# Kernel tuning notes

Measured on AMD Instinct MI355X. Metric: run time of the kernel, lower is better.

The kernel has to match this reference:

```python
import jax, jax.numpy as jnp
import numpy as np

N = 100_000          # nodes
E = 3_200_000        # train edges (avg degree 32)
E_TEST = 500_000     # pos/neg test edges each
F_IN, F_HID, F_OUT = 256, 16, 64


def setup_inputs() -> dict:
    key = jax.random.key(0)
    ks = jax.random.split(key, 7)
    x = jax.random.normal(ks[0], (N, F_IN), jnp.float32)
    train_edge_index = jax.random.randint(ks[1], (2, E), 0, N, dtype=jnp.int32)
    test_pos_edge_index = jax.random.randint(ks[2], (2, E_TEST), 0, N, dtype=jnp.int32)
    test_neg_edge_index = jax.random.randint(ks[3], (2, E_TEST), 0, N, dtype=jnp.int32)
    W1 = jax.random.normal(ks[4], (F_IN, F_HID), jnp.float32) / np.float32(np.sqrt(F_IN))
    b1 = jnp.zeros((F_HID,), jnp.float32)
    W2 = jax.random.normal(ks[5], (F_HID, F_OUT), jnp.float32) / np.float32(np.sqrt(F_HID))
    b2 = jnp.zeros((F_OUT,), jnp.float32)
    return dict(x=x, train_edge_index=train_edge_index,
                test_pos_edge_index=test_pos_edge_index,
                test_neg_edge_index=test_neg_edge_index,
                W1=W1, b1=b1, W2=W2, b2=b2)


def gcn_conv(x, edge_index, W, b, n):
    """PyG GCNConv: x' = D^-1/2 (A+I) D^-1/2 (x W) + b (self-loops added)."""
    h = x @ W                                  # project first (PyG order)
    loop = jnp.arange(n, dtype=edge_index.dtype)
    src = jnp.concatenate([edge_index[0], loop])
    dst = jnp.concatenate([edge_index[1], loop])
    deg = jax.ops.segment_sum(jnp.ones_like(dst, dtype=h.dtype), dst, num_segments=n)
    dinv = jnp.where(deg > 0, jax.lax.rsqrt(deg), 0.0)
    norm = dinv[src] * dinv[dst]               # per-edge symmetric norm
    msg = h[src] * norm[:, None]               # gather + scale
    out = jax.ops.segment_sum(msg, dst, num_segments=n)  # scatter-add
    return out + b


def reference(x, train_edge_index, test_pos_edge_index, test_neg_edge_index,
              W1, b1, W2, b2):
    n = x.shape[0]
    z = gcn_conv(x, train_edge_index, W1, b1, n)
    z = jax.nn.relu(z)
    z = gcn_conv(z, train_edge_index, W2, b2, n)
    edge_index = jnp.concatenate([test_pos_edge_index, test_neg_edge_index], axis=-1)
    logits = jnp.sum(z[edge_index[0]] * z[edge_index[1]], axis=-1)
    return logits
```

## Files before the change

### kernel.cpp

```cpp
#include <hip/hip_runtime.h>


#define NB_SHIFT 8
#define CAP   9728
#define CHUNK 8192

__global__ void seedprep_kernel(int* __restrict__ gtail, int nb1,
                                const float* __restrict__ W2, const float* __restrict__ b2,
                                float* __restrict__ mw) {
    int t = threadIdx.x;
    for (int i = t; i < nb1; i += 256) gtail[i] = i * CAP;
    int r = t >> 4, cc = t & 15;
    float s = 0.0f;
    for (int j = 0; j < 64; ++j) s += W2[r * 64 + j] * W2[cc * 64 + j];
    mw[t] = s;
    if (t < 16) {
        float w = 0.0f;
        for (int j = 0; j < 64; ++j) w += W2[t * 64 + j] * b2[j];
        mw[256 + t] = w;
    }
    if (t == 0) {
        float bbv = 0.0f;
        for (int j = 0; j < 64; ++j) bbv += b2[j] * b2[j];
        mw[272] = bbv;
    }
}

__global__ void __launch_bounds__(512)
passA1_kernel(const int* __restrict__ src, const int* __restrict__ dst, int E,
              int* __restrict__ gtail, unsigned* __restrict__ tmp, int nb1) {
    __shared__ int h[512];
    __shared__ int loff[512];
    __shared__ int cur[512];
    __shared__ int base[512];
    __shared__ unsigned srec[CHUNK];
    __shared__ unsigned short sbkt[CHUNK];
    int t = threadIdx.x;
    int c0 = blockIdx.x * CHUNK;
    int ce = min(CHUNK, E - c0);

    h[t] = 0;
    __syncthreads();
    for (int i = t; i < ce; i += 512)
        atomicAdd(&h[dst[c0 + i] >> NB_SHIFT], 1);
    __syncthreads();
    int cnt = h[t];
    loff[t] = cnt;
    __syncthreads();
    for (int off = 1; off < 512; off <<= 1) {
        int v = loff[t];
        int a = (t >= off) ? loff[t - off] : 0;
        __syncthreads();
        loff[t] = v + a;
        __syncthreads();
    }
    int excl = loff[t] - cnt;
    if (t < nb1) base[t] = atomicAdd(&gtail[t], cnt);
    loff[t] = excl;
    cur[t]  = excl;
    __syncthreads();
    for (int i = t; i < ce; i += 512) {
        int d = dst[c0 + i];
        int s = src[c0 + i];
        int b = d >> NB_SHIFT;
        int p = atomicAdd(&cur[b], 1);
        srec[p] = (unsigned)s | ((unsigned)(d & 255) << 20);
        sbkt[p] = (unsigned short)b;
    }
    __syncthreads();
    for (int i = t; i < ce; i += 512) {
        int b = sbkt[i];
        tmp[base[b] + (i - loff[b])] = srec[i];
    }
}

__global__ void __launch_bounds__(512)
fill2_kernel(const int* __restrict__ gtail, const unsigned* __restrict__ tmp,
             int* __restrict__ eidx, int* __restrict__ rowptr,
             int* __restrict__ counts, float* __restrict__ dinv, int n) {
    __shared__ int hh[256];
    __shared__ int sc[256];
    __shared__ int cur[256];
    __shared__ int sout[CAP];
    int b = blockIdx.x;
    int t = threadIdx.x;
    int beg = b * CAP;
    int cnt_total = gtail[b] - beg;

    if (t < 256) hh[t] = 0;
    __syncthreads();
    for (int i = t; i < cnt_total; i += 512)
        atomicAdd(&hh[tmp[beg + i] >> 20], 1);
    __syncthreads();
    if (t < 256) sc[t] = hh[t];
    __syncthreads();
    for (int off = 1; off < 256; off <<= 1) {
        int v = 0, a = 0;
        if (t < 256) { v = sc[t]; a = (t >= off) ? sc[t - off] : 0; }
        __syncthreads();
        if (t < 256) sc[t] = v + a;
        __syncthreads();
    }
    if (t < 256) {
        int ex = sc[t] - hh[t];
        cur[t] = ex;
        int v = (b << NB_SHIFT) + t;
        if (v < n) {
            rowptr[v] = beg + ex;
            counts[v] = hh[t];
            dinv[v]   = rsqrtf((float)hh[t] + 1.0f);
        }
    }
    __syncthreads();
    for (int i = t; i < cnt_total; i += 512) {
        unsigned r = tmp[beg + i];
        int p = atomicAdd(&cur[r >> 20], 1);
        sout[p] = (int)(r & 0xFFFFF);
    }
    __syncthreads();
    for (int i = t; i < cnt_total; i += 512)
        eidx[beg + i] = sout[i];
}

__global__ void __launch_bounds__(64)
gemm1_kernel(const float* __restrict__ x, const float* __restrict__ W1,
             const float* __restrict__ dinv, float* __restrict__ hs, int n) {
    int row = blockIdx.x * 64 + threadIdx.x;
    if (row >= n) return;
    const float4* x4 = (const float4*)(x + (size_t)row * 256);
    const float4* W14 = (const float4*)W1;
    float4 a0 = {0,0,0,0}, a1 = {0,0,0,0}, a2 = {0,0,0,0}, a3 = {0,0,0,0};
    float4 buf[8];
    #pragma unroll
    for (int j = 0; j < 8; ++j) buf[j] = x4[j];
    for (int k8 = 0; k8 < 8; ++k8) {
        float4 cur[8];
        #pragma unroll
        for (int j = 0; j < 8; ++j) cur[j] = buf[j];
        if (k8 < 7) {
            #pragma unroll
            for (int j = 0; j < 8; ++j) buf[j] = x4[(k8 + 1) * 8 + j];
        }
        #pragma unroll
        for (int jj = 0; jj < 8; ++jj) {
            float4 xv = cur[jj];
            int k4 = k8 * 8 + jj;
            #pragma unroll
            for (int j = 0; j < 4; ++j) {
                float xk = (j == 0) ? xv.x : (j == 1) ? xv.y : (j == 2) ? xv.z : xv.w;
                int k = (k4 << 2) + j;
                float4 w0 = W14[k * 4 + 0];
                float4 w1 = W14[k * 4 + 1];
                float4 w2 = W14[k * 4 + 2];
                float4 w3 = W14[k * 4 + 3];
                a0.x += xk * w0.x; a0.y += xk * w0.y; a0.z += xk * w0.z; a0.w += xk * w0.w;
                a1.x += xk * w1.x; a1.y += xk * w1.y; a1.z += xk * w1.z; a1.w += xk * w1.w;
                a2.x += xk * w2.x; a2.y += xk * w2.y; a2.z += xk * w2.z; a2.w += xk * w2.w;
                a3.x += xk * w3.x; a3.y += xk * w3.y; a3.z += xk * w3.z; a3.w += xk * w3.w;
            }
        }
    }
    float di = dinv[row];
    float4* o = (float4*)(hs + (size_t)row * 16);
    a0.x *= di; a0.y *= di; a0.z *= di; a0.w *= di;
    a1.x *= di; a1.y *= di; a1.z *= di; a1.w *= di;
    a2.x *= di; a2.y *= di; a2.z *= di; a2.w *= di;
    a3.x *= di; a3.y *= di; a3.z *= di; a3.w *= di;
    o[0] = a0; o[1] = a1; o[2] = a2; o[3] = a3;
}

__global__ void agg1_kernel(const int* __restrict__ rowptr, const int* __restrict__ counts,
                            const int* __restrict__ eidx, const float4* __restrict__ hs4,
                            const float* __restrict__ dinv, const float* __restrict__ b1,
                            float4* __restrict__ gs4, int n) {
    int t = blockIdx.x * blockDim.x + threadIdx.x;
    int v = t >> 3;
    if (v >= n) return;
    int q = t & 3, hh = (t >> 2) & 1;
    int start = rowptr[v], cnt = counts[v];
    float4 s = {0, 0, 0, 0};
    int i = hh;
    for (; i + 6 < cnt; i += 8) {
        int s0 = eidx[start + i];
        int s1 = eidx[start + i + 2];
        int s2 = eidx[start + i + 4];
        int s3 = eidx[start + i + 6];
        float4 h0 = hs4[(size_t)s0 * 4 + q];
        float4 h1 = hs4[(size_t)s1 * 4 + q];
        float4 h2 = hs4[(size_t)s2 * 4 + q];
        float4 h3 = hs4[(size_t)s3 * 4 + q];
        s.x += h0.x + h1.x + h2.x + h3.x;
        s.y += h0.y + h1.y + h2.y + h3.y;
        s.z += h0.z + h1.z + h2.z + h3.z;
        s.w += h0.w + h1.w + h2.w + h3.w;
    }
    for (; i < cnt; i += 2) {
        float4 h0 = hs4[(size_t)eidx[start + i] * 4 + q];
        s.x += h0.x; s.y += h0.y; s.z += h0.z; s.w += h0.w;
    }
    s.x += __shfl_xor(s.x, 4);
    s.y += __shfl_xor(s.y, 4);
    s.z += __shfl_xor(s.z, 4);
    s.w += __shfl_xor(s.w, 4);
    if (hh == 0) {
        float di = dinv[v];
        float4 h = hs4[(size_t)v * 4 + q];
        float4 b = ((const float4*)b1)[q];
        float4 z;
        z.x = fmaxf(di * (s.x + h.x) + b.x, 0.0f) * di;
        z.y = fmaxf(di * (s.y + h.y) + b.y, 0.0f) * di;
        z.z = fmaxf(di * (s.z + h.z) + b.z, 0.0f) * di;
        z.w = fmaxf(di * (s.w + h.w) + b.w, 0.0f) * di;
        gs4[(size_t)v * 4 + q] = z;
    }
}

__global__ void agg2y_kernel(const int* __restrict__ rowptr, const int* __restrict__ counts,
                             const int* __restrict__ eidx, const float4* __restrict__ gs4,
                             const float* __restrict__ dinv, const float* __restrict__ mw,
                             float4* __restrict__ u4, float* __restrict__ y,
                             float* __restrict__ c, int n) {
    __shared__ float su[32 * 16];
    __shared__ float sM[256];
    __shared__ float sw[16];
    int t = threadIdx.x;
    sM[t] = mw[t];
    if (t < 16) sw[t] = mw[256 + t];

    int j = t >> 3, q = t & 3, hh = (t >> 2) & 1;
    int v = blockIdx.x * 32 + j;
    if (v < n) {
        int start = rowptr[v], cnt = counts[v];
        float4 s = {0, 0, 0, 0};
        int i = hh;
        for (; i + 6 < cnt; i += 8) {
            int s0 = eidx[start + i];
            int s1 = eidx[start + i + 2];
            int s2 = eidx[start + i + 4];
            int s3 = eidx[start + i + 6];
            float4 g0 = gs4[(size_t)s0 * 4 + q];
            float4 g1 = gs4[(size_t)s1 * 4 + q];
            float4 g2 = gs4[(size_t)s2 * 4 + q];
            float4 g3 = gs4[(size_t)s3 * 4 + q];
            s.x += g0.x + g1.x + g2.x + g3.x;
            s.y += g0.y + g1.y + g2.y + g3.y;
            s.z += g0.z + g1.z + g2.z + g3.z;
            s.w += g0.w + g1.w + g2.w + g3.w;
        }
        for (; i < cnt; i += 2) {
            float4 g0 = gs4[(size_t)eidx[start + i] * 4 + q];
            s.x += g0.x; s.y += g0.y; s.z += g0.z; s.w += g0.w;
        }
        s.x += __shfl_xor(s.x, 4);
        s.y += __shfl_xor(s.y, 4);
        s.z += __shfl_xor(s.z, 4);
        s.w += __shfl_xor(s.w, 4);
        if (hh == 0) {
            float di = dinv[v];
            float4 g = gs4[(size_t)v * 4 + q];
            float4 uu;
            uu.x = di * (s.x + g.x);
            uu.y = di * (s.y + g.y);
            uu.z = di * (s.z + g.z);
            uu.w = di * (s.w + g.w);
            float* up = &su[j * 16 + q * 4];
            up[0] = uu.x; up[1] = uu.y; up[2] = uu.z; up[3] = uu.w;
            u4[(size_t)v * 4 + q] = uu;
        }
    }
    __syncthreads();
    if (v < n) {
        int l8 = t & 7;
        const float* uu = &su[j * 16];
        int c0 = l8 * 2;
        float y0 = sw[c0], y1 = sw[c0 + 1];
        #pragma unroll
        for (int k = 0; k < 16; ++k) {
            float uk = uu[k];
            y0 += uk * sM[k * 16 + c0];
            y1 += uk * sM[k * 16 + c0 + 1];
        }
        float2* yp = (float2*)(y + (size_t)v * 16 + c0);
        *yp = make_float2(y0, y1);
        if (l8 == 0) {
            float cv = 0.0f;
            #pragma unroll
            for (int k = 0; k < 16; ++k) cv += uu[k] * sw[k];
            c[v] = cv;
        }
    }
}

__global__ void edge_dot_kernel(const int* __restrict__ pa, const int* __restrict__ pb,
                                const int* __restrict__ na, const int* __restrict__ nb_,
                                int ET, const float* __restrict__ u, const float* __restrict__ y,
                                const float* __restrict__ c, const float* __restrict__ mw,
                                float* __restrict__ out) {
    int t = blockIdx.x * blockDim.x + threadIdx.x;
    int p = t >> 4, l = t & 15;
    if (p >= ET) return;
    int a0 = pa[p], b0 = pb[p];
    int a1 = na[p], b1 = nb_[p];
    float ya0 = y[(size_t)a0 * 16 + l];
    float ub0 = u[(size_t)b0 * 16 + l];
    float ya1 = y[(size_t)a1 * 16 + l];
    float ub1 = u[(size_t)b1 * 16 + l];
    float p0 = ya0 * ub0;
    float p1 = ya1 * ub1;
    p0 += __shfl_xor(p0, 1);  p1 += __shfl_xor(p1, 1);
    p0 += __shfl_xor(p0, 2);  p1 += __shfl_xor(p1, 2);
    p0 += __shfl_xor(p0, 4);  p1 += __shfl_xor(p1, 4);
    p0 += __shfl_xor(p0, 8);  p1 += __shfl_xor(p1, 8);
    if (l == 0) {
        float bb = mw[272];
        out[p]      = p0 + c[a0] + bb;
        out[ET + p] = p1 + c[a1] + bb;
    }
}

extern "C" void kernel_launch(void* const* d_in, const int* in_sizes, int n_in,
                              void* d_out, int out_size, void* d_ws, size_t ws_size,
                              hipStream_t stream) {
    const float* x    = (const float*)d_in[0];
    const int*   tei  = (const int*)d_in[1];
    const int*   tpos = (const int*)d_in[2];
    const int*   tneg = (const int*)d_in[3];
    const float* W1   = (const float*)d_in[4];
    const float* b1   = (const float*)d_in[5];
    const float* W2   = (const float*)d_in[6];
    const float* b2   = (const float*)d_in[7];
    float* out = (float*)d_out;

    int n   = in_sizes[0] / 256;
    int E   = in_sizes[1] / 2;
    int ET  = in_sizes[2] / 2;
    int nb1 = (n + 255) >> NB_SHIFT;

    char* w = (char*)d_ws;
    int*   gtail  = (int*)w;        w += 512 * 4;
    float* mw     = (float*)w;      w += 512 * 4;
    int*   rowptr = (int*)w;        w += (size_t)n * 4;
    int*   counts = (int*)w;        w += (size_t)n * 4;
    float* dinv   = (float*)w;      w += (size_t)n * 4;
    float* hs     = (float*)w;      w += (size_t)16 * n * 4;
    float* gs     = (float*)w;      w += (size_t)16 * n * 4;
    float* u      = (float*)w;      w += (size_t)16 * n * 4;
    float* y      = (float*)w;      w += (size_t)16 * n * 4;
    float* c      = (float*)w;      w += (size_t)n * 4;
    int*   eidx   = (int*)w;        w += (size_t)nb1 * CAP * 4;
    unsigned* tmp = (unsigned*)w;   w += (size_t)nb1 * CAP * 4;

    const int* src = tei;
    const int* dst = tei + E;

    seedprep_kernel<<<1, 256, 0, stream>>>(gtail, nb1, W2, b2, mw);
    passA1_kernel<<<(E + CHUNK - 1) / CHUNK, 512, 0, stream>>>(src, dst, E, gtail, tmp, nb1);
    fill2_kernel<<<nb1, 512, 0, stream>>>(gtail, tmp, eidx, rowptr, counts, dinv, n);

    gemm1_kernel<<<(n + 63) / 64, 64, 0, stream>>>(x, W1, dinv, hs, n);
    agg1_kernel<<<(8 * n + 255) / 256, 256, 0, stream>>>(rowptr, counts, eidx,
                                                         (const float4*)hs, dinv, b1,
                                                         (float4*)gs, n);
    agg2y_kernel<<<(n + 31) / 32, 256, 0, stream>>>(rowptr, counts, eidx,
                                                    (const float4*)gs, dinv, mw,
                                                    (float4*)u, y, c, n);
    edge_dot_kernel<<<(16 * ET + 255) / 256, 256, 0, stream>>>(tpos, tpos + ET, tneg, tneg + ET,
                                                               ET, u, y, c, mw, out);
}
```

Before: 349.6 us.

## Fuse dense projection into edge bucketing launch and defer dinv scaling to fill

The x@W1 projection no longer needs dinv, so it moves into the same launch as the edge bucketing pass, using separate block ranges so the bandwidth-heavy GEMM runs alongside the atomic-heavy partitioning. The dinv row scaling of hs moves to the end of fill2, where each block rescales its 256 rows in place using dinv values kept in shared memory. This removes one kernel launch and lets the two independent phases overlap. The cost is that GEMM blocks now use 512 threads and inherit the large shared-memory footprint of the partitioning blocks, which limits occupancy, and fill2 gains an extra read-modify-write pass over hs.

```diff
diff --git a/kernel.cpp b/kernel.cpp
--- a/kernel.cpp
+++ b/kernel.cpp
@@ -26,17 +26,60 @@
     }
 }
 
-__global__ void __launch_bounds__(512)
-passA1_kernel(const int* __restrict__ src, const int* __restrict__ dst, int E,
-              int* __restrict__ gtail, unsigned* __restrict__ tmp, int nb1) {
+__global__ void __launch_bounds__(512, 4)
+k1_kernel(const int* __restrict__ src, const int* __restrict__ dst, int E,
+          int* __restrict__ gtail, unsigned* __restrict__ tmp, int nb1,
+          const float* __restrict__ x, const float* __restrict__ W1,
+          float* __restrict__ hs, int n, int nblkG) {
+    int t = threadIdx.x;
+    if ((int)blockIdx.x < nblkG) {
+        int row = blockIdx.x * 512 + t;
+        if (row >= n) return;
+        const float4* x4 = (const float4*)(x + (size_t)row * 256);
+        const float4* W14 = (const float4*)W1;
+        float4 a0 = {0,0,0,0}, a1 = {0,0,0,0}, a2 = {0,0,0,0}, a3 = {0,0,0,0};
+        float4 buf[8];
+        #pragma unroll
+        for (int j = 0; j < 8; ++j) buf[j] = x4[j];
+        for (int k8 = 0; k8 < 8; ++k8) {
+            float4 cur[8];
+            #pragma unroll
+            for (int j = 0; j < 8; ++j) cur[j] = buf[j];
+            if (k8 < 7) {
+                #pragma unroll
+                for (int j = 0; j < 8; ++j) buf[j] = x4[(k8 + 1) * 8 + j];
+            }
+            #pragma unroll
+            for (int jj = 0; jj < 8; ++jj) {
+                float4 xv = cur[jj];
+                int k4 = k8 * 8 + jj;
+                #pragma unroll
+                for (int j = 0; j < 4; ++j) {
+                    float xk = (j == 0) ? xv.x : (j == 1) ? xv.y : (j == 2) ? xv.z : xv.w;
+                    int k = (k4 << 2) + j;
+                    float4 w0 = W14[k * 4 + 0];
+                    float4 w1 = W14[k * 4 + 1];
+                    float4 w2 = W14[k * 4 + 2];
+                    float4 w3 = W14[k * 4 + 3];
+                    a0.x += xk * w0.x; a0.y += xk * w0.y; a0.z += xk * w0.z; a0.w += xk * w0.w;
+                    a1.x += xk * w1.x; a1.y += xk * w1.y; a1.z += xk * w1.z; a1.w += xk * w1.w;
+                    a2.x += xk * w2.x; a2.y += xk * w2.y; a2.z += xk * w2.z; a2.w += xk * w2.w;
+                    a3.x += xk * w3.x; a3.y += xk * w3.y; a3.z += xk * w3.z; a3.w += xk * w3.w;
+                }
+            }
+        }
+        float4* o = (float4*)(hs + (size_t)row * 16);
+        o[0] = a0; o[1] = a1; o[2] = a2; o[3] = a3;
+        return;
+    }
+
     __shared__ int h[512];
     __shared__ int loff[512];
     __shared__ int cur[512];
     __shared__ int base[512];
     __shared__ unsigned srec[CHUNK];
     __shared__ unsigned short sbkt[CHUNK];
-    int t = threadIdx.x;
-    int c0 = blockIdx.x * CHUNK;
+    int c0 = (blockIdx.x - nblkG) * CHUNK;
     int ce = min(CHUNK, E - c0);
 
     h[t] = 0;
@@ -77,10 +120,12 @@
 __global__ void __launch_bounds__(512)
 fill2_kernel(const int* __restrict__ gtail, const unsigned* __restrict__ tmp,
              int* __restrict__ eidx, int* __restrict__ rowptr,
-             int* __restrict__ counts, float* __restrict__ dinv, int n) {
+             int* __restrict__ counts, float* __restrict__ dinv,
+             float* __restrict__ hs, int n) {
     __shared__ int hh[256];
     __shared__ int sc[256];
     __shared__ int cur[256];
+    __shared__ float sdinv[256];
     __shared__ int sout[CAP];
     int b = blockIdx.x;
     int t = threadIdx.x;
@@ -104,11 +149,13 @@
     if (t < 256) {
         int ex = sc[t] - hh[t];
         cur[t] = ex;
+        float dv = rsqrtf((float)hh[t] + 1.0f);
+        sdinv[t] = dv;
         int v = (b << NB_SHIFT) + t;
         if (v < n) {
             rowptr[v] = beg + ex;
             counts[v] = hh[t];
-            dinv[v]   = rsqrtf((float)hh[t] + 1.0f);
+            dinv[v]   = dv;
         }
     }
     __syncthreads();
@@ -120,53 +167,18 @@
     __syncthreads();
     for (int i = t; i < cnt_total; i += 512)
         eidx[beg + i] = sout[i];
-}
-
-__global__ void __launch_bounds__(64)
-gemm1_kernel(const float* __restrict__ x, const float* __restrict__ W1,
-             const float* __restrict__ dinv, float* __restrict__ hs, int n) {
-    int row = blockIdx.x * 64 + threadIdx.x;
-    if (row >= n) return;
-    const float4* x4 = (const float4*)(x + (size_t)row * 256);
-    const float4* W14 = (const float4*)W1;
-    float4 a0 = {0,0,0,0}, a1 = {0,0,0,0}, a2 = {0,0,0,0}, a3 = {0,0,0,0};
-    float4 buf[8];
-    #pragma unroll
-    for (int j = 0; j < 8; ++j) buf[j] = x4[j];
-    for (int k8 = 0; k8 < 8; ++k8) {
-        float4 cur[8];
-        #pragma unroll
-        for (int j = 0; j < 8; ++j) cur[j] = buf[j];
-        if (k8 < 7) {
-            #pragma unroll
-            for (int j = 0; j < 8; ++j) buf[j] = x4[(k8 + 1) * 8 + j];
-        }
-        #pragma unroll
-        for (int jj = 0; jj < 8; ++jj) {
-            float4 xv = cur[jj];
-            int k4 = k8 * 8 + jj;
-            #pragma unroll
-            for (int j = 0; j < 4; ++j) {
-                float xk = (j == 0) ? xv.x : (j == 1) ? xv.y : (j == 2) ? xv.z : xv.w;
-                int k = (k4 << 2) + j;
-                float4 w0 = W14[k * 4 + 0];
-                float4 w1 = W14[k * 4 + 1];
-                float4 w2 = W14[k * 4 + 2];
-                float4 w3 = W14[k * 4 + 3];
-                a0.x += xk * w0.x; a0.y += xk * w0.y; a0.z += xk * w0.z; a0.w += xk * w0.w;
-                a1.x += xk * w1.x; a1.y += xk * w1.y; a1.z += xk * w1.z; a1.w += xk * w1.w;
-                a2.x += xk * w2.x; a2.y += xk * w2.y; a2.z += xk * w2.z; a2.w += xk * w2.w;
-                a3.x += xk * w3.x; a3.y += xk * w3.y; a3.z += xk * w3.z; a3.w += xk * w3.w;
-            }
-        }
-    }
-    float di = dinv[row];
-    float4* o = (float4*)(hs + (size_t)row * 16);
-    a0.x *= di; a0.y *= di; a0.z *= di; a0.w *= di;
-    a1.x *= di; a1.y *= di; a1.z *= di; a1.w *= di;
-    a2.x *= di; a2.y *= di; a2.z *= di; a2.w *= di;
-    a3.x *= di; a3.y *= di; a3.z *= di; a3.w *= di;
-    o[0] = a0; o[1] = a1; o[2] = a2; o[3] = a3;
+    int v0 = b << NB_SHIFT;
+    int rows = min(256, n - v0);
+    if (rows > 0) {
+        float4* h4 = (float4*)(hs + (size_t)v0 * 16);
+        int tot = rows * 4;
+        for (int i = t; i < tot; i += 512) {
+            float4 hv = h4[i];
+            float dv = sdinv[i >> 2];
+            hv.x *= dv; hv.y *= dv; hv.z *= dv; hv.w *= dv;
+            h4[i] = hv;
+        }
+    }
 }
 
 __global__ void agg1_kernel(const int* __restrict__ rowptr, const int* __restrict__ counts,
@@ -353,11 +365,14 @@
     const int* src = tei;
     const int* dst = tei + E;
 
+    int nblkA = (E + CHUNK - 1) / CHUNK;
+    int nblkG = (n + 511) / 512;
+
     seedprep_kernel<<<1, 256, 0, stream>>>(gtail, nb1, W2, b2, mw);
-    passA1_kernel<<<(E + CHUNK - 1) / CHUNK, 512, 0, stream>>>(src, dst, E, gtail, tmp, nb1);
-    fill2_kernel<<<nb1, 512, 0, stream>>>(gtail, tmp, eidx, rowptr, counts, dinv, n);
-
-    gemm1_kernel<<<(n + 63) / 64, 64, 0, stream>>>(x, W1, dinv, hs, n);
+    k1_kernel<<<nblkG + nblkA, 512, 0, stream>>>(src, dst, E, gtail, tmp, nb1,
+                                                 x, W1, hs, n, nblkG);
+    fill2_kernel<<<nb1, 512, 0, stream>>>(gtail, tmp, eidx, rowptr, counts, dinv, hs, n);
+
     agg1_kernel<<<(8 * n + 255) / 256, 256, 0, stream>>>(rowptr, counts, eidx,
                                                          (const float4*)hs, dinv, b1,
                                                          (float4*)gs, n);
```

After: 343.8 us. No clear change (-1.6%).
